# Optimization experiments

Hardware: AMD Instinct MI355X
Metric: run time of the kernel (lower is better)

## Reference

```python
import jax, jax.numpy as jnp
import numpy as np
import math

D_MODEL = 2048
B, S, PAST = 4, 2048, 2048


def setup_inputs() -> dict:
    key = jax.random.key(0)
    ks = jax.random.split(key, 8)
    scale = 0.02
    x = jax.random.normal(ks[0], (B, S, D_MODEL), dtype=jnp.float32)
    past_k = jax.random.normal(ks[1], (B, PAST, D_MODEL), dtype=jnp.float32)
    past_v = jax.random.normal(ks[2], (B, PAST, D_MODEL), dtype=jnp.float32)
    Wq = jax.random.normal(ks[3], (D_MODEL, D_MODEL), dtype=jnp.float32) * scale
    Wk = jax.random.normal(ks[4], (D_MODEL, D_MODEL), dtype=jnp.float32) * scale
    Wv = jax.random.normal(ks[5], (D_MODEL, D_MODEL), dtype=jnp.float32) * scale
    Wo = jax.random.normal(ks[6], (D_MODEL, D_MODEL), dtype=jnp.float32) * scale
    bq = jnp.zeros((D_MODEL,), jnp.float32)
    bk = jnp.zeros((D_MODEL,), jnp.float32)
    bv = jnp.zeros((D_MODEL,), jnp.float32)
    bo = jnp.zeros((D_MODEL,), jnp.float32)
    return {"x": x, "past_k": past_k, "past_v": past_v,
            "Wq": Wq, "bq": bq, "Wk": Wk, "bk": bk,
            "Wv": Wv, "bv": bv, "Wo": Wo, "bo": bo}


def reference(x, past_k, past_v, Wq, bq, Wk, bk, Wv, bv, Wo, bo):
    d_model = x.shape[-1]
    # torch Linear: y = x @ W.T + b; here W is stored [out, in] equivalently square
    q = jnp.einsum('bsd,ed->bse', x, Wq) + bq
    k = jnp.einsum('bsd,ed->bse', x, Wk) + bk
    v = jnp.einsum('bsd,ed->bse', x, Wv) + bv
    k_cache = jnp.concatenate([past_k, k], axis=1)  # [B, PAST+S, D]
    v_cache = jnp.concatenate([past_v, v], axis=1)
    scores = jnp.einsum('bqd,bkd->bqk', q, k_cache) / math.sqrt(d_model)
    weights = jax.nn.softmax(scores, axis=-1)
    attn = jnp.einsum('bqk,bkd->bqd', weights, v_cache)
    out = jnp.einsum('bqd,ed->bqe', attn, Wo) + bo
    return out, (k_cache, v_cache)
```

## Files before the change

kernel.cpp:

```cpp
#include <hip/hip_runtime.h>
#include <math.h>

typedef unsigned short u16;
typedef __bf16 bf16x8 __attribute__((ext_vector_type(8)));
typedef float f32x4 __attribute__((ext_vector_type(4)));
typedef short s16x8 __attribute__((ext_vector_type(8)));

#define DM 2048
#define NB 4
#define SEQ 2048
#define PAST_N 2048
#define CS 4096

__device__ __forceinline__ u16 f2bf(float f) {
  unsigned u = __float_as_uint(f);
  u += 0x7fff + ((u >> 16) & 1);
  return (u16)(u >> 16);
}
__device__ __forceinline__ float bf2f(u16 h) {
  return __uint_as_float(((unsigned)h) << 16);
}

__device__ __forceinline__ void gl_lds16(const u16* g, u16* l) {
  __builtin_amdgcn_global_load_lds(
      (const __attribute__((address_space(1))) unsigned*)g,
      (__attribute__((address_space(3))) unsigned*)l, 16, 0, 0);
}

__device__ __forceinline__ void stage_op(const u16* __restrict__ g, int ld,
                                         int ko, u16* sl, int w, int lr, int kh) {
#pragma unroll
  for (int j = 0; j < 2; ++j) {
    const int u = w * 2 + j;
    gl_lds16(g + (long)(u * 16 + lr) * ld + ko + kh * 8, sl + u * 512);
  }
}

template <int EPI, bool REMAP>
__global__ __launch_bounds__(512, 2) void gemm256(
    const u16* __restrict__ A, const u16* __restrict__ B,
    float* __restrict__ Cf, u16* __restrict__ Cb, const float* __restrict__ bias,
    int K, int lda, int ldb, int ldc, long strA, long strB, long strC,
    float scale) {
  __shared__ __align__(16) u16 shA[3][256 * 32];
  __shared__ __align__(16) u16 shB[3][256 * 32];
  const int t = threadIdx.x;
  const int lane = t & 63;
  const int w = t >> 6;
  const int wr = w >> 2, wc = w & 3;
  const int lr = lane & 15, kh = lane >> 4;

  const int gx = gridDim.x, gy = gridDim.y;
  const int nwg = gx * gy * gridDim.z;
  const int orig = blockIdx.x + gx * (blockIdx.y + gy * blockIdx.z);
  const int swz = (orig & 7) * (nwg >> 3) + (orig >> 3);
  const int bx = swz % gx;
  const int r1 = swz / gx;
  const int by = r1 % gy;
  const long bz = r1 / gy;
  const int brow = by * 256, bcol = bx * 256;

  const u16* Ab = A + bz * strA + (long)brow * lda;
  const u16* Bb = B + bz * strB + (long)bcol * ldb;

  const int NT = K >> 5;

  stage_op(Ab, lda, 0, shA[0], w, lr, kh);
  stage_op(Bb, ldb, 0, shB[0], w, lr, kh);
  if (NT > 1) {
    stage_op(Ab, lda, 32, shA[1], w, lr, kh);
    stage_op(Bb, ldb, 32, shB[1], w, lr, kh);
  }

  f32x4 acc[8][4] = {};
  bf16x8 a[4], b[4];

  for (int tt = 0; tt < NT; ++tt) {
    const int slot = tt % 3;
    const u16* sA = shA[slot];
    const u16* sB = shB[slot];
    const int ns = (tt + 2) % 3;
    const bool st = (tt + 2 < NT);
    const int ko = (tt + 2) << 5;

    if (tt + 1 < NT)
      asm volatile("s_waitcnt vmcnt(4)" ::: "memory");
    else
      asm volatile("s_waitcnt vmcnt(0)" ::: "memory");
    __builtin_amdgcn_s_barrier();
    __builtin_amdgcn_sched_barrier(0);

#pragma unroll
    for (int mi = 0; mi < 4; ++mi)
      a[mi] = *(const bf16x8*)(sA + (wr * 8 + mi) * 512 + lane * 8);
#pragma unroll
    for (int ni = 0; ni < 4; ++ni)
      b[ni] = *(const bf16x8*)(sB + (wc * 4 + ni) * 512 + lane * 8);
    if (st) stage_op(Ab, lda, ko, shA[ns], w, lr, kh);
    __builtin_amdgcn_s_barrier();
    asm volatile("s_waitcnt lgkmcnt(0)" ::: "memory");
    __builtin_amdgcn_sched_barrier(0);
    __builtin_amdgcn_s_setprio(1);
#pragma unroll
    for (int mi = 0; mi < 4; ++mi)
#pragma unroll
      for (int ni = 0; ni < 4; ++ni)
        acc[mi][ni] = __builtin_amdgcn_mfma_f32_16x16x32_bf16(
            a[mi], b[ni], acc[mi][ni], 0, 0, 0);
    __builtin_amdgcn_s_setprio(0);
    __builtin_amdgcn_s_barrier();

#pragma unroll
    for (int mi = 0; mi < 4; ++mi)
      a[mi] = *(const bf16x8*)(sA + (wr * 8 + 4 + mi) * 512 + lane * 8);
    if (st) stage_op(Bb, ldb, ko, shB[ns], w, lr, kh);
    asm volatile("s_waitcnt lgkmcnt(0)" ::: "memory");
    __builtin_amdgcn_sched_barrier(0);
    __builtin_amdgcn_s_setprio(1);
#pragma unroll
    for (int mi = 0; mi < 4; ++mi)
#pragma unroll
      for (int ni = 0; ni < 4; ++ni)
        acc[4 + mi][ni] = __builtin_amdgcn_mfma_f32_16x16x32_bf16(
            a[mi], b[ni], acc[4 + mi][ni], 0, 0, 0);
    __builtin_amdgcn_s_setprio(0);
  }

  const long cb = bz * strC;
#pragma unroll
  for (int mi = 0; mi < 8; ++mi) {
    const int r0 = wr * 128 + mi * 16 + kh * 4;
#pragma unroll
    for (int ni = 0; ni < 4; ++ni) {
      const int c = bcol + wc * 64 + ni * 16 + lr;
      const float bv = bias ? bias[c] : 0.0f;
#pragma unroll
      for (int r = 0; r < 4; ++r) {
        const int row = brow + r0 + r;
        const long orow = REMAP ? (long)((row >> 11) * CS + PAST_N + (row & (SEQ - 1)))
                                : (long)row;
        const float val = (acc[mi][ni][r] + bv) * scale;
        if (EPI == 0 || EPI == 2) Cf[cb + orow * (long)ldc + c] = val;
        if (EPI == 1 || EPI == 2) Cb[cb + orow * (long)ldc + c] = f2bf(val);
      }
    }
  }
}

__global__ __launch_bounds__(256) void cast_bf16_kn(const float* __restrict__ in,
                                                    u16* __restrict__ out) {
  const int i = blockIdx.x * 256 + threadIdx.x;
  const float4 v = ((const float4*)in)[i];
  ushort4 o;
  o.x = f2bf(v.x); o.y = f2bf(v.y); o.z = f2bf(v.z); o.w = f2bf(v.w);
  ((ushort4*)out)[i] = o;
}

__global__ __launch_bounds__(256) void copy_past_kv(const float* __restrict__ pk,
                                                    const float* __restrict__ pv,
                                                    float* __restrict__ kc,
                                                    float* __restrict__ vc,
                                                    u16* __restrict__ kb) {
  const int i = blockIdx.x * 256 + threadIdx.x;
  const int d4 = DM / 4;
  const int row = i / d4;
  const int col = i - row * d4;
  const int bb = row >> 11, p = row & (PAST_N - 1);
  const long o = ((long)(bb * CS + p)) * d4 + col;
  if (blockIdx.z == 0) {
    const float4 v = ((const float4*)pk)[i];
    ((float4*)kc)[o] = v;
    ushort4 u;
    u.x = f2bf(v.x); u.y = f2bf(v.y); u.z = f2bf(v.z); u.w = f2bf(v.w);
    ((ushort4*)kb)[o] = u;
  } else {
    ((float4*)vc)[o] = ((const float4*)pv)[i];
  }
}

__global__ __launch_bounds__(256) void transpose_cast(const float* __restrict__ vcache,
                                                      u16* __restrict__ vt) {
  __shared__ float tile[32][33];
  const int bb = blockIdx.z;
  const int k0 = blockIdx.x * 32, d0 = blockIdx.y * 32;
  const int tx = threadIdx.x & 31, ty = threadIdx.x >> 5;
  const float* src = vcache + (long)bb * CS * DM;
#pragma unroll
  for (int j = 0; j < 4; ++j)
    tile[ty + 8 * j][tx] = src[(long)(k0 + ty + 8 * j) * DM + d0 + tx];
  __syncthreads();
  u16* dst = vt + (long)bb * DM * CS;
#pragma unroll
  for (int j = 0; j < 4; ++j)
    dst[(long)(d0 + ty + 8 * j) * CS + k0 + tx] = f2bf(tile[tx][ty + 8 * j]);
}

__global__ __launch_bounds__(256) void softmax_rows(u16* __restrict__ s) {
  const long row = blockIdx.x;
  u16* p = s + row * CS;
  const int t = threadIdx.x;
  const int lane = t & 63, w = t >> 6;
  float v[16];
  s16x8 c0 = ((const s16x8*)p)[t * 2];
  s16x8 c1 = ((const s16x8*)p)[t * 2 + 1];
#pragma unroll
  for (int i = 0; i < 8; ++i) {
    v[i] = bf2f((u16)c0[i]);
    v[8 + i] = bf2f((u16)c1[i]);
  }
  float m = v[0];
#pragma unroll
  for (int i = 1; i < 16; ++i) m = fmaxf(m, v[i]);
#pragma unroll
  for (int o = 32; o >= 1; o >>= 1) m = fmaxf(m, __shfl_xor(m, o, 64));
  __shared__ float red[4];
  if (lane == 0) red[w] = m;
  __syncthreads();
  m = fmaxf(fmaxf(red[0], red[1]), fmaxf(red[2], red[3]));
  float sum = 0.f;
#pragma unroll
  for (int i = 0; i < 16; ++i) {
    v[i] = __expf(v[i] - m);
    sum += v[i];
  }
#pragma unroll
  for (int o = 32; o >= 1; o >>= 1) sum += __shfl_xor(sum, o, 64);
  __syncthreads();
  if (lane == 0) red[w] = sum;
  __syncthreads();
  sum = red[0] + red[1] + red[2] + red[3];
  const float inv = 1.0f / sum;
#pragma unroll
  for (int i = 0; i < 8; ++i) {
    c0[i] = (short)f2bf(v[i] * inv);
    c1[i] = (short)f2bf(v[8 + i] * inv);
  }
  ((s16x8*)p)[t * 2] = c0;
  ((s16x8*)p)[t * 2 + 1] = c1;
}

extern "C" void kernel_launch(void* const* d_in, const int* in_sizes, int n_in,
                              void* d_out, int out_size, void* d_ws, size_t ws_size,
                              hipStream_t stream) {
  const float* x  = (const float*)d_in[0];
  const float* pk = (const float*)d_in[1];
  const float* pv = (const float*)d_in[2];
  const float* Wq = (const float*)d_in[3];
  const float* bq = (const float*)d_in[4];
  const float* Wk = (const float*)d_in[5];
  const float* bk = (const float*)d_in[6];
  const float* Wv = (const float*)d_in[7];
  const float* bv = (const float*)d_in[8];
  const float* Wo = (const float*)d_in[9];
  const float* bo = (const float*)d_in[10];

  float* out = (float*)d_out;
  float* kc = out + (long)NB * SEQ * DM;
  float* vc = kc + (long)NB * CS * DM;

  u16* ws = (u16*)d_ws;
  u16* xb  = ws;
  u16* wqb = ws + 16777216;
  u16* wkb = wqb + 4194304;
  u16* wvb = wkb + 4194304;
  u16* wob = wvb + 4194304;
  u16* qb  = ws + 33554432;
  u16* kb  = ws + 50331648;
  u16* vtb = ws + 83886080;
  u16* sc  = ws + 117440512;

  const float qscale = 0.022097086912079608f;

  cast_bf16_kn<<<16384, 256, 0, stream>>>(x, xb);
  cast_bf16_kn<<<4096, 256, 0, stream>>>(Wq, wqb);
  cast_bf16_kn<<<4096, 256, 0, stream>>>(Wk, wkb);
  cast_bf16_kn<<<4096, 256, 0, stream>>>(Wv, wvb);
  cast_bf16_kn<<<4096, 256, 0, stream>>>(Wo, wob);

  gemm256<1, false><<<dim3(8, 32, 1), 512, 0, stream>>>(
      xb, wqb, nullptr, qb, bq, 2048, 2048, 2048, 2048, 0, 0, 0, qscale);
  gemm256<2, true><<<dim3(8, 32, 1), 512, 0, stream>>>(
      xb, wkb, kc, kb, bk, 2048, 2048, 2048, 2048, 0, 0, 0, 1.0f);
  gemm256<0, true><<<dim3(8, 32, 1), 512, 0, stream>>>(
      xb, wvb, vc, nullptr, bv, 2048, 2048, 2048, 2048, 0, 0, 0, 1.0f);

  copy_past_kv<<<dim3(16384, 1, 2), 256, 0, stream>>>(pk, pv, kc, vc, kb);

  transpose_cast<<<dim3(128, 64, 4), 256, 0, stream>>>(vc, vtb);

  gemm256<1, false><<<dim3(16, 8, 4), 512, 0, stream>>>(
      qb, kb, nullptr, sc, nullptr, 2048, 2048, 2048, 4096,
      2048L * 2048, 4096L * 2048, 2048L * 4096, 1.0f);

  softmax_rows<<<8192, 256, 0, stream>>>(sc);

  gemm256<1, false><<<dim3(8, 8, 4), 512, 0, stream>>>(
      sc, vtb, nullptr, xb, nullptr, 4096, 4096, 4096, 2048,
      2048L * 4096, 2048L * 4096, 2048L * 2048, 1.0f);

  gemm256<0, false><<<dim3(8, 32, 1), 512, 0, stream>>>(
      xb, wob, out, nullptr, bo, 2048, 2048, 2048, 2048, 0, 0, 0, 1.0f);
}
```

Measured before the change: 819.9 us.

## Software-pipeline GEMM main loop with register double-buffering and fewer barriers

Rewrites the bf16 MFMA GEMM inner loop to unroll by two k-tiles and prefetch LDS fragments for the next half-step or tile into separate register sets while the current MFMAs run. Synchronisation drops to one waitcnt plus barrier per k-tile, replacing the two barriers per tile used before. The aim is to overlap LDS reads with MFMA work and cut barrier stalls. In exchange, each gate now waits for all outstanding global loads (vmcnt(0)), which shortens the effective prefetch depth. The code also assumes the tile count is even and at least two, and uses more registers.

```diff
diff --git a/kernel.cpp b/kernel.cpp
--- a/kernel.cpp
+++ b/kernel.cpp
@@ -35,6 +35,26 @@
     gl_lds16(g + (long)(u * 16 + lr) * ld + ko + kh * 8, sl + u * 512);
   }
 }
+
+#define RD_A(dst, sAp, ph)                                              \
+  _Pragma("unroll") for (int mi = 0; mi < 4; ++mi)                      \
+      dst[mi] = *(const bf16x8*)((sAp) + (wr * 8 + (ph) * 4 + mi) * 512 + lane * 8);
+#define RD_B(dst, sBp)                                                  \
+  _Pragma("unroll") for (int ni = 0; ni < 4; ++ni)                      \
+      dst[ni] = *(const bf16x8*)((sBp) + (wc * 4 + ni) * 512 + lane * 8);
+
+#define MMC(lo, fa, fb)                                                 \
+  __builtin_amdgcn_s_setprio(1);                                        \
+  _Pragma("unroll") for (int mi = 0; mi < 4; ++mi)                      \
+  _Pragma("unroll") for (int ni = 0; ni < 4; ++ni)                      \
+      acc[(lo) + mi][ni] = __builtin_amdgcn_mfma_f32_16x16x32_bf16(     \
+          fa[mi], fb[ni], acc[(lo) + mi][ni], 0, 0, 0);                 \
+  __builtin_amdgcn_s_setprio(0);
+
+#define GATE()                                                          \
+  asm volatile("s_waitcnt vmcnt(0)" ::: "memory");                      \
+  __builtin_amdgcn_s_barrier();                                         \
+  __builtin_amdgcn_sched_barrier(0);
 
 template <int EPI, bool REMAP>
 __global__ __launch_bounds__(512, 2) void gemm256(
@@ -67,63 +87,62 @@
 
   stage_op(Ab, lda, 0, shA[0], w, lr, kh);
   stage_op(Bb, ldb, 0, shB[0], w, lr, kh);
-  if (NT > 1) {
-    stage_op(Ab, lda, 32, shA[1], w, lr, kh);
-    stage_op(Bb, ldb, 32, shB[1], w, lr, kh);
-  }
+  stage_op(Ab, lda, 32, shA[1], w, lr, kh);
+  stage_op(Bb, ldb, 32, shB[1], w, lr, kh);
+  asm volatile("s_waitcnt vmcnt(4)" ::: "memory");
+  __builtin_amdgcn_s_barrier();
+  __builtin_amdgcn_sched_barrier(0);
 
   f32x4 acc[8][4] = {};
-  bf16x8 a[4], b[4];
-
-  for (int tt = 0; tt < NT; ++tt) {
-    const int slot = tt % 3;
-    const u16* sA = shA[slot];
-    const u16* sB = shB[slot];
-    const int ns = (tt + 2) % 3;
-    const bool st = (tt + 2 < NT);
-    const int ko = (tt + 2) << 5;
-
-    if (tt + 1 < NT)
-      asm volatile("s_waitcnt vmcnt(4)" ::: "memory");
-    else
-      asm volatile("s_waitcnt vmcnt(0)" ::: "memory");
-    __builtin_amdgcn_s_barrier();
-    __builtin_amdgcn_sched_barrier(0);
-
-#pragma unroll
-    for (int mi = 0; mi < 4; ++mi)
-      a[mi] = *(const bf16x8*)(sA + (wr * 8 + mi) * 512 + lane * 8);
-#pragma unroll
-    for (int ni = 0; ni < 4; ++ni)
-      b[ni] = *(const bf16x8*)(sB + (wc * 4 + ni) * 512 + lane * 8);
-    if (st) stage_op(Ab, lda, ko, shA[ns], w, lr, kh);
-    __builtin_amdgcn_s_barrier();
-    asm volatile("s_waitcnt lgkmcnt(0)" ::: "memory");
-    __builtin_amdgcn_sched_barrier(0);
-    __builtin_amdgcn_s_setprio(1);
-#pragma unroll
-    for (int mi = 0; mi < 4; ++mi)
-#pragma unroll
-      for (int ni = 0; ni < 4; ++ni)
-        acc[mi][ni] = __builtin_amdgcn_mfma_f32_16x16x32_bf16(
-            a[mi], b[ni], acc[mi][ni], 0, 0, 0);
-    __builtin_amdgcn_s_setprio(0);
-    __builtin_amdgcn_s_barrier();
-
-#pragma unroll
-    for (int mi = 0; mi < 4; ++mi)
-      a[mi] = *(const bf16x8*)(sA + (wr * 8 + 4 + mi) * 512 + lane * 8);
-    if (st) stage_op(Bb, ldb, ko, shB[ns], w, lr, kh);
-    asm volatile("s_waitcnt lgkmcnt(0)" ::: "memory");
-    __builtin_amdgcn_sched_barrier(0);
-    __builtin_amdgcn_s_setprio(1);
-#pragma unroll
-    for (int mi = 0; mi < 4; ++mi)
-#pragma unroll
-      for (int ni = 0; ni < 4; ++ni)
-        acc[4 + mi][ni] = __builtin_amdgcn_mfma_f32_16x16x32_bf16(
-            a[mi], b[ni], acc[4 + mi][ni], 0, 0, 0);
-    __builtin_amdgcn_s_setprio(0);
+  bf16x8 ea[4], eb[4], oa[4], ob[4], p1[4];
+
+  RD_A(ea, shA[0], 0)
+  RD_B(eb, shB[0])
+
+  int s0 = 0;
+  for (int tp = 0; tp + 2 < NT; tp += 2) {
+    const int s1 = (s0 + 1 == 3) ? 0 : s0 + 1;
+    const int s2 = (s1 + 1 == 3) ? 0 : s1 + 1;
+    const u16* sA0 = shA[s0];
+    const u16* sA1 = shA[s1];
+    const u16* sB1 = shB[s1];
+    const u16* sA2 = shA[s2];
+    const u16* sB2 = shB[s2];
+
+    RD_A(p1, sA0, 1)
+    MMC(0, ea, eb)
+    GATE()
+    stage_op(Ab, lda, (tp + 2) << 5, shA[s2], w, lr, kh);
+    stage_op(Bb, ldb, (tp + 2) << 5, shB[s2], w, lr, kh);
+    RD_A(oa, sA1, 0)
+    RD_B(ob, sB1)
+    MMC(4, p1, eb)
+    RD_A(p1, sA1, 1)
+    MMC(0, oa, ob)
+    GATE()
+    stage_op(Ab, lda, (tp + 3) << 5, shA[s0], w, lr, kh);
+    stage_op(Bb, ldb, (tp + 3) << 5, shB[s0], w, lr, kh);
+    RD_A(ea, sA2, 0)
+    RD_B(eb, sB2)
+    MMC(4, p1, ob)
+
+    s0 = s2;
+  }
+
+  {
+    const int s1 = (s0 + 1 == 3) ? 0 : s0 + 1;
+    const u16* sA0 = shA[s0];
+    const u16* sA1 = shA[s1];
+    const u16* sB1 = shB[s1];
+    RD_A(p1, sA0, 1)
+    MMC(0, ea, eb)
+    GATE()
+    RD_A(oa, sA1, 0)
+    RD_B(ob, sB1)
+    MMC(4, p1, eb)
+    RD_A(p1, sA1, 1)
+    MMC(0, oa, ob)
+    MMC(4, p1, ob)
   }
 
   const long cb = bz * strC;
```

After: 1.021 ms. 24.6% more time.

## Deepen GEMM LDS pipeline to four stages with peeled epilogue tiles

Applied to the files above, without the earlier changes.

Grows the shared-memory ring from three to four K-tile slots, so three tiles are prefetched up front. The vmcnt wait moves to the end of each iteration, and the last three tiles become a peeled epilogue with no stage loads. The goal is to hide more global-to-LDS latency behind the MFMA work and to drop the per-iteration conditional staging. In exchange LDS use per block rises to 128KB, and the kernel now assumes K covers at least four tiles.

```diff
diff --git a/kernel.cpp b/kernel.cpp
--- a/kernel.cpp
+++ b/kernel.cpp
@@ -35,6 +35,44 @@
     gl_lds16(g + (long)(u * 16 + lr) * ld + ko + kh * 8, sl + u * 512);
   }
 }
+
+#define RD_A(dst, sAp, ph)                                              \
+  _Pragma("unroll") for (int mi = 0; mi < 4; ++mi)                      \
+      dst[mi] = *(const bf16x8*)((sAp) + (wr * 8 + (ph) * 4 + mi) * 512 + lane * 8);
+#define RD_B(dst, sBp)                                                  \
+  _Pragma("unroll") for (int ni = 0; ni < 4; ++ni)                      \
+      dst[ni] = *(const bf16x8*)((sBp) + (wc * 4 + ni) * 512 + lane * 8);
+
+#define MMC(lo, fa, fb)                                                 \
+  __builtin_amdgcn_s_setprio(1);                                        \
+  _Pragma("unroll") for (int mi = 0; mi < 4; ++mi)                      \
+  _Pragma("unroll") for (int ni = 0; ni < 4; ++ni)                      \
+      acc[(lo) + mi][ni] = __builtin_amdgcn_mfma_f32_16x16x32_bf16(     \
+          fa[mi], fb[ni], acc[(lo) + mi][ni], 0, 0, 0);                 \
+  __builtin_amdgcn_s_setprio(0);
+
+#define PHASE_FENCE                                                     \
+  __builtin_amdgcn_s_barrier();                                         \
+  asm volatile("s_waitcnt lgkmcnt(0)" ::: "memory");                    \
+  __builtin_amdgcn_sched_barrier(0);
+
+#define TILE_NOSTAGE(ttv, GATE_STMT)                                    \
+  do {                                                                  \
+    const int slot_ = (ttv) & 3;                                        \
+    const u16* sA_ = shA[slot_];                                        \
+    const u16* sB_ = shB[slot_];                                        \
+    RD_A(a, sA_, 0)                                                     \
+    RD_B(b, sB_)                                                        \
+    PHASE_FENCE                                                         \
+    MMC(0, a, b)                                                        \
+    __builtin_amdgcn_s_barrier();                                       \
+    RD_A(a, sA_, 1)                                                     \
+    asm volatile("s_waitcnt lgkmcnt(0)" ::: "memory");                  \
+    __builtin_amdgcn_sched_barrier(0);                                  \
+    MMC(4, a, b)                                                        \
+    GATE_STMT;                                                          \
+    __builtin_amdgcn_s_barrier();                                       \
+  } while (0)
 
 template <int EPI, bool REMAP>
 __global__ __launch_bounds__(512, 2) void gemm256(
@@ -42,8 +80,8 @@
     float* __restrict__ Cf, u16* __restrict__ Cb, const float* __restrict__ bias,
     int K, int lda, int ldb, int ldc, long strA, long strB, long strC,
     float scale) {
-  __shared__ __align__(16) u16 shA[3][256 * 32];
-  __shared__ __align__(16) u16 shB[3][256 * 32];
+  __shared__ __align__(16) u16 shA[4][256 * 32];
+  __shared__ __align__(16) u16 shB[4][256 * 32];
   const int t = threadIdx.x;
   const int lane = t & 63;
   const int w = t >> 6;
@@ -67,64 +105,42 @@
 
   stage_op(Ab, lda, 0, shA[0], w, lr, kh);
   stage_op(Bb, ldb, 0, shB[0], w, lr, kh);
-  if (NT > 1) {
-    stage_op(Ab, lda, 32, shA[1], w, lr, kh);
-    stage_op(Bb, ldb, 32, shB[1], w, lr, kh);
-  }
+  stage_op(Ab, lda, 32, shA[1], w, lr, kh);
+  stage_op(Bb, ldb, 32, shB[1], w, lr, kh);
+  stage_op(Ab, lda, 64, shA[2], w, lr, kh);
+  stage_op(Bb, ldb, 64, shB[2], w, lr, kh);
+  asm volatile("s_waitcnt vmcnt(8)" ::: "memory");
+  __builtin_amdgcn_s_barrier();
+  __builtin_amdgcn_sched_barrier(0);
 
   f32x4 acc[8][4] = {};
   bf16x8 a[4], b[4];
 
-  for (int tt = 0; tt < NT; ++tt) {
-    const int slot = tt % 3;
+  for (int tt = 0; tt < NT - 3; ++tt) {
+    const int slot = tt & 3, s3 = (tt + 3) & 3;
     const u16* sA = shA[slot];
     const u16* sB = shB[slot];
-    const int ns = (tt + 2) % 3;
-    const bool st = (tt + 2 < NT);
-    const int ko = (tt + 2) << 5;
-
-    if (tt + 1 < NT)
-      asm volatile("s_waitcnt vmcnt(4)" ::: "memory");
-    else
-      asm volatile("s_waitcnt vmcnt(0)" ::: "memory");
+    const int ko = (tt + 3) << 5;
+
+    RD_A(a, sA, 0)
+    RD_B(b, sB)
+    stage_op(Ab, lda, ko, shA[s3], w, lr, kh);
+    PHASE_FENCE
+    MMC(0, a, b)
     __builtin_amdgcn_s_barrier();
-    __builtin_amdgcn_sched_barrier(0);
-
-#pragma unroll
-    for (int mi = 0; mi < 4; ++mi)
-      a[mi] = *(const bf16x8*)(sA + (wr * 8 + mi) * 512 + lane * 8);
-#pragma unroll
-    for (int ni = 0; ni < 4; ++ni)
-      b[ni] = *(const bf16x8*)(sB + (wc * 4 + ni) * 512 + lane * 8);
-    if (st) stage_op(Ab, lda, ko, shA[ns], w, lr, kh);
-    __builtin_amdgcn_s_barrier();
+
+    RD_A(a, sA, 1)
+    stage_op(Bb, ldb, ko, shB[s3], w, lr, kh);
     asm volatile("s_waitcnt lgkmcnt(0)" ::: "memory");
     __builtin_amdgcn_sched_barrier(0);
-    __builtin_amdgcn_s_setprio(1);
-#pragma unroll
-    for (int mi = 0; mi < 4; ++mi)
-#pragma unroll
-      for (int ni = 0; ni < 4; ++ni)
-        acc[mi][ni] = __builtin_amdgcn_mfma_f32_16x16x32_bf16(
-            a[mi], b[ni], acc[mi][ni], 0, 0, 0);
-    __builtin_amdgcn_s_setprio(0);
+    MMC(4, a, b)
+    asm volatile("s_waitcnt vmcnt(8)" ::: "memory");
     __builtin_amdgcn_s_barrier();
-
-#pragma unroll
-    for (int mi = 0; mi < 4; ++mi)
-      a[mi] = *(const bf16x8*)(sA + (wr * 8 + 4 + mi) * 512 + lane * 8);
-    if (st) stage_op(Bb, ldb, ko, shB[ns], w, lr, kh);
-    asm volatile("s_waitcnt lgkmcnt(0)" ::: "memory");
-    __builtin_amdgcn_sched_barrier(0);
-    __builtin_amdgcn_s_setprio(1);
-#pragma unroll
-    for (int mi = 0; mi < 4; ++mi)
-#pragma unroll
-      for (int ni = 0; ni < 4; ++ni)
-        acc[4 + mi][ni] = __builtin_amdgcn_mfma_f32_16x16x32_bf16(
-            a[mi], b[ni], acc[4 + mi][ni], 0, 0, 0);
-    __builtin_amdgcn_s_setprio(0);
-  }
+  }
+
+  TILE_NOSTAGE(NT - 3, asm volatile("s_waitcnt vmcnt(4)" ::: "memory"));
+  TILE_NOSTAGE(NT - 2, asm volatile("s_waitcnt vmcnt(0)" ::: "memory"));
+  TILE_NOSTAGE(NT - 1, );
 
   const long cb = bz * strC;
 #pragma unroll
```

Result: slower. 963.2 us (+17.5%).

## Shrink GEMM tiles to 128x128 with double-buffered LDS and 4 waves

Applied to the files above, without the earlier changes.

Replaces the 256x256, 8-wave, triple-buffered GEMM with a 128x128, 4-wave, double-buffered version and launches four times as many workgroups. The simpler pipeline drops the split A/B staging, setprio hints and intermediate barriers. It is meant to raise occupancy and grid size. In exchange, operand reuse per LDS load is lower, global traffic per FLOP is higher, and less load/compute overlap is possible.

```diff
diff --git a/kernel.cpp b/kernel.cpp
--- a/kernel.cpp
+++ b/kernel.cpp
@@ -37,17 +37,17 @@
 }
 
 template <int EPI, bool REMAP>
-__global__ __launch_bounds__(512, 2) void gemm256(
+__global__ __launch_bounds__(256, 4) void gemm128(
     const u16* __restrict__ A, const u16* __restrict__ B,
     float* __restrict__ Cf, u16* __restrict__ Cb, const float* __restrict__ bias,
     int K, int lda, int ldb, int ldc, long strA, long strB, long strC,
     float scale) {
-  __shared__ __align__(16) u16 shA[3][256 * 32];
-  __shared__ __align__(16) u16 shB[3][256 * 32];
+  __shared__ __align__(16) u16 shA[2][128 * 32];
+  __shared__ __align__(16) u16 shB[2][128 * 32];
   const int t = threadIdx.x;
   const int lane = t & 63;
   const int w = t >> 6;
-  const int wr = w >> 2, wc = w & 3;
+  const int wr = w >> 1, wc = w & 1;
   const int lr = lane & 15, kh = lane >> 4;
 
   const int gx = gridDim.x, gy = gridDim.y;
@@ -58,7 +58,7 @@
   const int r1 = swz / gx;
   const int by = r1 % gy;
   const long bz = r1 / gy;
-  const int brow = by * 256, bcol = bx * 256;
+  const int brow = by * 128, bcol = bx * 128;
 
   const u16* Ab = A + bz * strA + (long)brow * lda;
   const u16* Bb = B + bz * strB + (long)bcol * ldb;
@@ -67,23 +67,18 @@
 
   stage_op(Ab, lda, 0, shA[0], w, lr, kh);
   stage_op(Bb, ldb, 0, shB[0], w, lr, kh);
-  if (NT > 1) {
-    stage_op(Ab, lda, 32, shA[1], w, lr, kh);
-    stage_op(Bb, ldb, 32, shB[1], w, lr, kh);
-  }
-
-  f32x4 acc[8][4] = {};
+  stage_op(Ab, lda, 32, shA[1], w, lr, kh);
+  stage_op(Bb, ldb, 32, shB[1], w, lr, kh);
+
+  f32x4 acc[4][4] = {};
   bf16x8 a[4], b[4];
 
   for (int tt = 0; tt < NT; ++tt) {
-    const int slot = tt % 3;
-    const u16* sA = shA[slot];
-    const u16* sB = shB[slot];
-    const int ns = (tt + 2) % 3;
-    const bool st = (tt + 2 < NT);
-    const int ko = (tt + 2) << 5;
-
-    if (tt + 1 < NT)
+    const int cur = tt & 1;
+    const u16* sA = shA[cur];
+    const u16* sB = shB[cur];
+
+    if (tt < NT - 1)
       asm volatile("s_waitcnt vmcnt(4)" ::: "memory");
     else
       asm volatile("s_waitcnt vmcnt(0)" ::: "memory");
@@ -92,44 +87,30 @@
 
 #pragma unroll
     for (int mi = 0; mi < 4; ++mi)
-      a[mi] = *(const bf16x8*)(sA + (wr * 8 + mi) * 512 + lane * 8);
+      a[mi] = *(const bf16x8*)(sA + (wr * 4 + mi) * 512 + lane * 8);
 #pragma unroll
     for (int ni = 0; ni < 4; ++ni)
       b[ni] = *(const bf16x8*)(sB + (wc * 4 + ni) * 512 + lane * 8);
-    if (st) stage_op(Ab, lda, ko, shA[ns], w, lr, kh);
-    __builtin_amdgcn_s_barrier();
-    asm volatile("s_waitcnt lgkmcnt(0)" ::: "memory");
-    __builtin_amdgcn_sched_barrier(0);
-    __builtin_amdgcn_s_setprio(1);
+
 #pragma unroll
     for (int mi = 0; mi < 4; ++mi)
 #pragma unroll
       for (int ni = 0; ni < 4; ++ni)
         acc[mi][ni] = __builtin_amdgcn_mfma_f32_16x16x32_bf16(
             a[mi], b[ni], acc[mi][ni], 0, 0, 0);
-    __builtin_amdgcn_s_setprio(0);
+
     __builtin_amdgcn_s_barrier();
-
-#pragma unroll
-    for (int mi = 0; mi < 4; ++mi)
-      a[mi] = *(const bf16x8*)(sA + (wr * 8 + 4 + mi) * 512 + lane * 8);
-    if (st) stage_op(Bb, ldb, ko, shB[ns], w, lr, kh);
-    asm volatile("s_waitcnt lgkmcnt(0)" ::: "memory");
-    __builtin_amdgcn_sched_barrier(0);
-    __builtin_amdgcn_s_setprio(1);
-#pragma unroll
-    for (int mi = 0; mi < 4; ++mi)
-#pragma unroll
-      for (int ni = 0; ni < 4; ++ni)
-        acc[4 + mi][ni] = __builtin_amdgcn_mfma_f32_16x16x32_bf16(
-            a[mi], b[ni], acc[4 + mi][ni], 0, 0, 0);
-    __builtin_amdgcn_s_setprio(0);
+    if (tt + 2 < NT) {
+      const int ko = (tt + 2) << 5;
+      stage_op(Ab, lda, ko, shA[cur], w, lr, kh);
+      stage_op(Bb, ldb, ko, shB[cur], w, lr, kh);
+    }
   }
 
   const long cb = bz * strC;
 #pragma unroll
-  for (int mi = 0; mi < 8; ++mi) {
-    const int r0 = wr * 128 + mi * 16 + kh * 4;
+  for (int mi = 0; mi < 4; ++mi) {
+    const int r0 = wr * 64 + mi * 16 + kh * 4;
 #pragma unroll
     for (int ni = 0; ni < 4; ++ni) {
       const int c = bcol + wc * 64 + ni * 16 + lr;
@@ -277,27 +258,27 @@
   cast_bf16_kn<<<4096, 256, 0, stream>>>(Wv, wvb);
   cast_bf16_kn<<<4096, 256, 0, stream>>>(Wo, wob);
 
-  gemm256<1, false><<<dim3(8, 32, 1), 512, 0, stream>>>(
+  gemm128<1, false><<<dim3(16, 64, 1), 256, 0, stream>>>(
       xb, wqb, nullptr, qb, bq, 2048, 2048, 2048, 2048, 0, 0, 0, qscale);
-  gemm256<2, true><<<dim3(8, 32, 1), 512, 0, stream>>>(
+  gemm128<2, true><<<dim3(16, 64, 1), 256, 0, stream>>>(
       xb, wkb, kc, kb, bk, 2048, 2048, 2048, 2048, 0, 0, 0, 1.0f);
-  gemm256<0, true><<<dim3(8, 32, 1), 512, 0, stream>>>(
+  gemm128<0, true><<<dim3(16, 64, 1), 256, 0, stream>>>(
       xb, wvb, vc, nullptr, bv, 2048, 2048, 2048, 2048, 0, 0, 0, 1.0f);
 
   copy_past_kv<<<dim3(16384, 1, 2), 256, 0, stream>>>(pk, pv, kc, vc, kb);
 
   transpose_cast<<<dim3(128, 64, 4), 256, 0, stream>>>(vc, vtb);
 
-  gemm256<1, false><<<dim3(16, 8, 4), 512, 0, stream>>>(
+  gemm128<1, false><<<dim3(32, 16, 4), 256, 0, stream>>>(
       qb, kb, nullptr, sc, nullptr, 2048, 2048, 2048, 4096,
       2048L * 2048, 4096L * 2048, 2048L * 4096, 1.0f);
 
   softmax_rows<<<8192, 256, 0, stream>>>(sc);
 
-  gemm256<1, false><<<dim3(8, 8, 4), 512, 0, stream>>>(
+  gemm128<1, false><<<dim3(16, 16, 4), 256, 0, stream>>>(
       sc, vtb, nullptr, xb, nullptr, 4096, 4096, 4096, 2048,
       2048L * 4096, 2048L * 4096, 2048L * 2048, 1.0f);
 
-  gemm256<0, false><<<dim3(8, 32, 1), 512, 0, stream>>>(
+  gemm128<0, false><<<dim3(16, 64, 1), 256, 0, stream>>>(
       xb, wob, out, nullptr, bo, 2048, 2048, 2048, 2048, 0, 0, 0, 1.0f);
 }
```

Measured after the change: 1.221 ms. 49.0% more time.
